# Performance work log

Hardware: AMD Instinct MI355X
Metric: run time of the kernel (lower is better)

The kernel has to match this reference:

```python
import jax, jax.numpy as jnp
import numpy as np

BLOCK_SIZE = 512
EPS = 1e-06


def setup_inputs() -> dict:
    key = jax.random.key(0)
    k1, k2, k3 = jax.random.split(key, 3)
    B, H, S, D = 2, 32, 4096, 128
    return {
        "query_states": jax.random.normal(k1, (B, H, S, D), dtype=jnp.float32),
        "key_states": jax.random.normal(k2, (B, H, S, D), dtype=jnp.float32),
        "value_states": jax.random.normal(k3, (B, H, S, D), dtype=jnp.float32),
        "phi_scale": jnp.ones((H, 1, D), dtype=jnp.float32),
        "phi_bias": jnp.zeros((H, 1, D), dtype=jnp.float32),
    }


def _feature_map(x, phi_scale, phi_bias):
    # x: (B, H, N, S_blk, D); scale/bias: (H, 1, D) -> broadcast over (B, N)
    y = x * phi_scale[None, :, None] + phi_bias[None, :, None]
    return jax.nn.elu(y) + 1.0


def reference(query_states, key_states, value_states, phi_scale, phi_bias):
    B, H, S, D = query_states.shape
    nb = (S + BLOCK_SIZE - 1) // BLOCK_SIZE
    pad = nb * BLOCK_SIZE - S
    if pad > 0:
        p = [(0, 0), (0, 0), (0, pad), (0, 0)]
        query_states = jnp.pad(query_states, p)
        key_states = jnp.pad(key_states, p)
        value_states = jnp.pad(value_states, p)
    q = query_states.reshape(B, H, nb, BLOCK_SIZE, D)
    k = key_states.reshape(B, H, nb, BLOCK_SIZE, D)
    v = value_states.reshape(B, H, nb, BLOCK_SIZE, D)
    phi_q = _feature_map(q, phi_scale, phi_bias)
    phi_k = _feature_map(k, phi_scale, phi_bias)
    # per-block KV aggregation: S_dm = sum_s phi_k[s,d] v[s,m]
    S_dm = jnp.einsum('bhnsd,bhnsm->bhndm', phi_k, v)
    Z = phi_k.sum(axis=-2)  # (B, H, nb, D)
    num = jnp.einsum('bhnsd,bhndm->bhnsm', phi_q, S_dm)
    den = jnp.einsum('bhnsd,bhnd->bhns', phi_q, Z)[..., None] + EPS
    out = (num / den).reshape(B, H, nb * BLOCK_SIZE, D)
    if pad > 0:
        out = out[:, :, :S, :]
    return out
```

## Files before the change

### kernel.cpp

```cpp
#include <hip/hip_runtime.h>
#include <cstdint>

#define NH 32
#define SEQ 4096
#define DDIM 128
#define BSZ 512
#define SKC 64
#define NCH 8
#define KT_STRIDE 33
#define ST_STRIDE 68
#define OFF_K0 0
#define OFF_V0 (128 * KT_STRIDE)
#define OFF_K1 (2 * 128 * KT_STRIDE)
#define OFF_V1 (3 * 128 * KT_STRIDE)
#define OFF_ST 0
#define OFF_QS0 (128 * ST_STRIDE)
#define OFF_QS1 (OFF_QS0 + 64 * ST_STRIDE)
#define OFF_Z   (OFF_QS1 + 64 * ST_STRIDE)
#define OFF_DEN0 (OFF_Z + 128)
#define OFF_DEN1 (OFF_DEN0 + 64)
#define LDS_DW (OFF_DEN1 + 64)

typedef _Float16 f16x8 __attribute__((ext_vector_type(8)));
typedef float f32x4 __attribute__((ext_vector_type(4)));

union FragU { uint32_t u[4]; f16x8 v; };

__device__ __forceinline__ float phi_fn(float x, float s, float b) {
    float y = fmaf(x, s, b);
    return y > 0.0f ? (y + 1.0f) : __expf(y);
}

__device__ __forceinline__ uint32_t pack_f16(float a, float b) {
    union { _Float16 h[2]; uint32_t u; } p;
    p.h[0] = (_Float16)a;
    p.h[1] = (_Float16)b;
    return p.u;
}

__global__ __launch_bounds__(256, 2) void linattn_kernel(
    const float* __restrict__ qg, const float* __restrict__ kg,
    const float* __restrict__ vg, const float* __restrict__ psg,
    const float* __restrict__ pbg, float* __restrict__ outg)
{
    __shared__ uint32_t lds[LDS_DW];
    float*    ldsf = (float*)lds;
    _Float16* ldsh = (_Float16*)lds;

    const int tid  = threadIdx.x;
    const int lane = tid & 63;
    const int wv   = tid >> 6;
    const int l15  = lane & 15;
    const int qd   = lane >> 4;

    const int gid = blockIdx.x;
    const int nb  = gid & 7;
    const int hh  = (gid >> 3) & 31;
    const int bb  = gid >> 8;

    const size_t base = ((size_t)(bb * NH + hh) * SEQ + (size_t)nb * BSZ) * DDIM;

    const int dp = tid & 63;
    const int qt = tid >> 6;
    const float2 sc2 = *(const float2*)(psg + hh * DDIM + 2 * dp);
    const float2 bi2 = *(const float2*)(pbg + hh * DDIM + 2 * dp);

    const int d4  = (tid & 31) * 4;
    const int sl2 = tid >> 5;
    const float4 sc4 = *(const float4*)(psg + hh * DDIM + d4);
    const float4 bi4 = *(const float4*)(pbg + hh * DDIM + d4);

    if (tid < 128) ldsf[OFF_Z + tid] = 0.0f;

    float z0 = 0.0f, z1 = 0.0f;

    f32x4 acc[2][8];
    #pragma unroll
    for (int a = 0; a < 2; ++a)
        #pragma unroll
        for (int c = 0; c < 8; ++c)
            acc[a][c] = (f32x4){0.f, 0.f, 0.f, 0.f};

    float2 kr[16], vr[16];
    const float* kbase = kg + base + 2 * dp;
    const float* vbase = vg + base + 2 * dp;

    auto loadkv = [&](int ch) {
        const size_t off = (size_t)(ch * SKC + qt * 16) * DDIM;
        #pragma unroll
        for (int j = 0; j < 16; ++j) {
            kr[j] = *(const float2*)(kbase + off + (size_t)j * DDIM);
            vr[j] = *(const float2*)(vbase + off + (size_t)j * DDIM);
        }
    };
    auto stagekv = [&](int buf) {
        uint32_t* bk = lds + (buf ? OFF_K1 : OFF_K0) + qt * 8;
        uint32_t* bv = lds + (buf ? OFF_V1 : OFF_V0) + qt * 8;
        const int r0 = (2 * dp) * KT_STRIDE;
        const int r1 = r0 + KT_STRIDE;
        #pragma unroll
        for (int j = 0; j < 8; ++j) {
            float p0x = phi_fn(kr[2*j].x,   sc2.x, bi2.x);
            float p1x = phi_fn(kr[2*j+1].x, sc2.x, bi2.x);
            float p0y = phi_fn(kr[2*j].y,   sc2.y, bi2.y);
            float p1y = phi_fn(kr[2*j+1].y, sc2.y, bi2.y);
            z0 += p0x + p1x;
            z1 += p0y + p1y;
            bk[r0 + j] = pack_f16(p0x, p1x);
            bk[r1 + j] = pack_f16(p0y, p1y);
            bv[r0 + j] = pack_f16(vr[2*j].x, vr[2*j+1].x);
            bv[r1 + j] = pack_f16(vr[2*j].y, vr[2*j+1].y);
        }
    };
    auto mfma1 = [&](int buf) {
        const int offK = buf ? OFF_K1 : OFF_K0;
        const int offV = buf ? OFF_V1 : OFF_V0;
        #pragma unroll
        for (int ks = 0; ks < 2; ++ks) {
            FragU af[2];
            #pragma unroll
            for (int tm = 0; tm < 2; ++tm) {
                const int m  = wv * 32 + tm * 16 + l15;
                const int ad = offV + m * KT_STRIDE + ks * 16 + qd * 4;
                af[tm].u[0] = lds[ad + 0]; af[tm].u[1] = lds[ad + 1];
                af[tm].u[2] = lds[ad + 2]; af[tm].u[3] = lds[ad + 3];
            }
            #pragma unroll
            for (int td = 0; td < 8; ++td) {
                const int dd = td * 16 + l15;
                const int bd = offK + dd * KT_STRIDE + ks * 16 + qd * 4;
                FragU bf;
                bf.u[0] = lds[bd + 0]; bf.u[1] = lds[bd + 1];
                bf.u[2] = lds[bd + 2]; bf.u[3] = lds[bd + 3];
                acc[0][td] = __builtin_amdgcn_mfma_f32_16x16x32_f16(af[0].v, bf.v, acc[0][td], 0, 0, 0);
                acc[1][td] = __builtin_amdgcn_mfma_f32_16x16x32_f16(af[1].v, bf.v, acc[1][td], 0, 0, 0);
            }
        }
    };

    loadkv(0);
    stagekv(0);
    loadkv(1);
    __syncthreads();
    for (int ch = 0; ch < NCH; ++ch) {
        if (ch + 1 < NCH) stagekv((ch + 1) & 1);
        if (ch + 2 < NCH) loadkv(ch + 2);
        mfma1(ch & 1);
        __syncthreads();
    }

    atomicAdd(&ldsf[OFF_Z + 2 * dp],     z0);
    atomicAdd(&ldsf[OFF_Z + 2 * dp + 1], z1);

    #pragma unroll
    for (int tm = 0; tm < 2; ++tm)
        #pragma unroll
        for (int td = 0; td < 8; ++td)
            #pragma unroll
            for (int r = 0; r < 4; ++r) {
                const int m  = wv * 32 + tm * 16 + qd * 4 + r;
                const int dd = td * 16 + l15;
                ldsh[m * (ST_STRIDE * 2) + dd] = (_Float16)acc[tm][td][r];
            }
    __syncthreads();

    const float4 zq = *(const float4*)(ldsf + OFF_Z + d4);

    float4 qr[8];
    const float* qbase = qg + base + d4;

    auto loadq = [&](int qc) {
        const size_t off = (size_t)(qc * SKC) * DDIM;
        #pragma unroll
        for (int i = 0; i < 8; ++i)
            qr[i] = *(const float4*)(qbase + off + (size_t)(sl2 + i * 8) * DDIM);
    };
    auto stageq = [&](int buf) {
        uint32_t* qsb  = lds  + (buf ? OFF_QS1  : OFF_QS0);
        float*    denb = ldsf + (buf ? OFF_DEN1 : OFF_DEN0);
        #pragma unroll
        for (int i = 0; i < 8; ++i) {
            const int srow = sl2 + i * 8;
            float p0 = phi_fn(qr[i].x, sc4.x, bi4.x);
            float p1 = phi_fn(qr[i].y, sc4.y, bi4.y);
            float p2 = phi_fn(qr[i].z, sc4.z, bi4.z);
            float p3 = phi_fn(qr[i].w, sc4.w, bi4.w);
            uint2 w;
            w.x = pack_f16(p0, p1);
            w.y = pack_f16(p2, p3);
            *(uint2*)(qsb + srow * ST_STRIDE + (tid & 31) * 2) = w;
            float pd = p0 * zq.x + p1 * zq.y + p2 * zq.z + p3 * zq.w;
            pd += __shfl_xor(pd, 16);
            pd += __shfl_xor(pd, 8);
            pd += __shfl_xor(pd, 4);
            pd += __shfl_xor(pd, 2);
            pd += __shfl_xor(pd, 1);
            if ((tid & 31) == 0) denb[srow] = pd;
        }
    };

    loadq(0);
    stageq(0);
    loadq(1);
    __syncthreads();

    for (int qc = 0; qc < 8; ++qc) {
        if (qc + 1 < 8) stageq((qc + 1) & 1);
        if (qc + 2 < 8) loadq(qc + 2);

        f32x4 acc2[8];
        #pragma unroll
        for (int c = 0; c < 8; ++c) acc2[c] = (f32x4){0.f, 0.f, 0.f, 0.f};

        const int qsOff  = (qc & 1) ? OFF_QS1  : OFF_QS0;
        const int denOff = (qc & 1) ? OFF_DEN1 : OFF_DEN0;

        #pragma unroll
        for (int ks = 0; ks < 4; ++ks) {
            const int srow = wv * 16 + l15;
            const int ad = qsOff + srow * ST_STRIDE + ks * 16 + qd * 4;
            FragU af;
            const uint4 t0 = *(const uint4*)(lds + ad);
            af.u[0] = t0.x; af.u[1] = t0.y; af.u[2] = t0.z; af.u[3] = t0.w;
            #pragma unroll
            for (int tn = 0; tn < 8; ++tn) {
                const int mm = tn * 16 + l15;
                const uint4 t1 = *(const uint4*)(lds + OFF_ST + mm * ST_STRIDE + ks * 16 + qd * 4);
                FragU bf;
                bf.u[0] = t1.x; bf.u[1] = t1.y; bf.u[2] = t1.z; bf.u[3] = t1.w;
                acc2[tn] = __builtin_amdgcn_mfma_f32_16x16x32_f16(af.v, bf.v, acc2[tn], 0, 0, 0);
            }
        }

        #pragma unroll
        for (int r = 0; r < 4; ++r) {
            const int srow = wv * 16 + qd * 4 + r;
            const float rden = 1.0f / (ldsf[denOff + srow] + 1e-6f);
            float* op = outg + base + (size_t)(qc * SKC + srow) * DDIM;
            #pragma unroll
            for (int tn = 0; tn < 8; ++tn)
                __builtin_nontemporal_store(acc2[tn][r] * rden, op + tn * 16 + l15);
        }
        if (qc + 1 < 8) __syncthreads();
    }
}

extern "C" void kernel_launch(void* const* d_in, const int* in_sizes, int n_in,
                              void* d_out, int out_size, void* d_ws, size_t ws_size,
                              hipStream_t stream) {
    const float* q  = (const float*)d_in[0];
    const float* k  = (const float*)d_in[1];
    const float* v  = (const float*)d_in[2];
    const float* ps = (const float*)d_in[3];
    const float* pb = (const float*)d_in[4];
    float* out = (float*)d_out;
    linattn_kernel<<<dim3(512), dim3(256), 0, stream>>>(q, k, v, ps, pb, out);
}
```

Baseline: 403.6 us.

## Use 512-thread blocks, swizzled K/V LDS layout, and register-direct Q phase

Block size goes from 256 to 512 threads, so each wave accumulates one 16-row tile of the K^T V product instead of two. The padded K/V LDS tiles become XOR-swizzled 32-dword rows with 128-bit stores and fragment loads. The Q phase no longer stages phi(q) in LDS: each wave loads its Q rows straight into MFMA fragments, computes the denominator with shuffles, and drops the per-chunk barriers and double buffering. The aim is more waves per CU, fewer LDS bank conflicts and instructions, and less synchronisation, at the cost of losing explicit prefetch of Q loads.

```diff
diff --git a/kernel.cpp b/kernel.cpp
--- a/kernel.cpp
+++ b/kernel.cpp
@@ -7,19 +7,17 @@
 #define BSZ 512
 #define SKC 64
 #define NCH 8
-#define KT_STRIDE 33
 #define ST_STRIDE 68
+
 #define OFF_K0 0
-#define OFF_V0 (128 * KT_STRIDE)
-#define OFF_K1 (2 * 128 * KT_STRIDE)
-#define OFF_V1 (3 * 128 * KT_STRIDE)
+#define OFF_V0 4096
+#define OFF_K1 8192
+#define OFF_V1 12288
 #define OFF_ST 0
-#define OFF_QS0 (128 * ST_STRIDE)
-#define OFF_QS1 (OFF_QS0 + 64 * ST_STRIDE)
-#define OFF_Z   (OFF_QS1 + 64 * ST_STRIDE)
-#define OFF_DEN0 (OFF_Z + 128)
-#define OFF_DEN1 (OFF_DEN0 + 64)
-#define LDS_DW (OFF_DEN1 + 64)
+#define OFF_Z  16384
+#define OFF_SC 16512
+#define OFF_SB 16640
+#define LDS_DW 16768
 
 typedef _Float16 f16x8 __attribute__((ext_vector_type(8)));
 typedef float f32x4 __attribute__((ext_vector_type(4)));
@@ -38,7 +36,7 @@
     return p.u;
 }
 
-__global__ __launch_bounds__(256, 2) void linattn_kernel(
+__global__ __launch_bounds__(512, 4) void linattn_kernel(
     const float* __restrict__ qg, const float* __restrict__ kg,
     const float* __restrict__ vg, const float* __restrict__ psg,
     const float* __restrict__ pbg, float* __restrict__ outg)
@@ -60,80 +58,83 @@
 
     const size_t base = ((size_t)(bb * NH + hh) * SEQ + (size_t)nb * BSZ) * DDIM;
 
-    const int dp = tid & 63;
-    const int qt = tid >> 6;
+    if (tid < 32) {
+        *(f32x4*)(ldsf + OFF_SC + tid * 4) = *(const f32x4*)(psg + hh * DDIM + tid * 4);
+    } else if (tid < 64) {
+        *(f32x4*)(ldsf + OFF_SB + (tid - 32) * 4) = *(const f32x4*)(pbg + hh * DDIM + (tid - 32) * 4);
+    }
+    if (tid < 128) ldsf[OFF_Z + tid] = 0.0f;
+
+    const int dp = lane;
     const float2 sc2 = *(const float2*)(psg + hh * DDIM + 2 * dp);
     const float2 bi2 = *(const float2*)(pbg + hh * DDIM + 2 * dp);
 
-    const int d4  = (tid & 31) * 4;
-    const int sl2 = tid >> 5;
-    const float4 sc4 = *(const float4*)(psg + hh * DDIM + d4);
-    const float4 bi4 = *(const float4*)(pbg + hh * DDIM + d4);
-
-    if (tid < 128) ldsf[OFF_Z + tid] = 0.0f;
-
     float z0 = 0.0f, z1 = 0.0f;
 
-    f32x4 acc[2][8];
+    f32x4 acc[8];
     #pragma unroll
-    for (int a = 0; a < 2; ++a)
-        #pragma unroll
-        for (int c = 0; c < 8; ++c)
-            acc[a][c] = (f32x4){0.f, 0.f, 0.f, 0.f};
-
-    float2 kr[16], vr[16];
+    for (int c = 0; c < 8; ++c) acc[c] = (f32x4){0.f, 0.f, 0.f, 0.f};
+
+    float2 kr[8], vr[8];
     const float* kbase = kg + base + 2 * dp;
     const float* vbase = vg + base + 2 * dp;
 
     auto loadkv = [&](int ch) {
-        const size_t off = (size_t)(ch * SKC + qt * 16) * DDIM;
-        #pragma unroll
-        for (int j = 0; j < 16; ++j) {
+        const size_t off = (size_t)(ch * SKC + wv * 8) * DDIM;
+        #pragma unroll
+        for (int j = 0; j < 8; ++j) {
             kr[j] = *(const float2*)(kbase + off + (size_t)j * DDIM);
             vr[j] = *(const float2*)(vbase + off + (size_t)j * DDIM);
         }
     };
+
     auto stagekv = [&](int buf) {
-        uint32_t* bk = lds + (buf ? OFF_K1 : OFF_K0) + qt * 8;
-        uint32_t* bv = lds + (buf ? OFF_V1 : OFF_V0) + qt * 8;
-        const int r0 = (2 * dp) * KT_STRIDE;
-        const int r1 = r0 + KT_STRIDE;
+        uint32_t* bk = lds + (buf ? OFF_K1 : OFF_K0);
+        uint32_t* bv = lds + (buf ? OFF_V1 : OFF_V0);
+        const int blk = ((wv ^ (dp & 7)) << 2);
+        uint32_t* k0 = bk + (2 * dp) * 32 + blk;
+        uint32_t* k1 = k0 + 32;
+        uint32_t* v0 = bv + (2 * dp) * 32 + blk;
+        uint32_t* v1 = v0 + 32;
+        float px[8], py[8];
         #pragma unroll
         for (int j = 0; j < 8; ++j) {
-            float p0x = phi_fn(kr[2*j].x,   sc2.x, bi2.x);
-            float p1x = phi_fn(kr[2*j+1].x, sc2.x, bi2.x);
-            float p0y = phi_fn(kr[2*j].y,   sc2.y, bi2.y);
-            float p1y = phi_fn(kr[2*j+1].y, sc2.y, bi2.y);
-            z0 += p0x + p1x;
-            z1 += p0y + p1y;
-            bk[r0 + j] = pack_f16(p0x, p1x);
-            bk[r1 + j] = pack_f16(p0y, p1y);
-            bv[r0 + j] = pack_f16(vr[2*j].x, vr[2*j+1].x);
-            bv[r1 + j] = pack_f16(vr[2*j].y, vr[2*j+1].y);
-        }
+            px[j] = phi_fn(kr[j].x, sc2.x, bi2.x);
+            py[j] = phi_fn(kr[j].y, sc2.y, bi2.y);
+            z0 += px[j];
+            z1 += py[j];
+        }
+        uint4 a;
+        a.x = pack_f16(px[0], px[1]); a.y = pack_f16(px[2], px[3]);
+        a.z = pack_f16(px[4], px[5]); a.w = pack_f16(px[6], px[7]);
+        *(uint4*)k0 = a;
+        a.x = pack_f16(py[0], py[1]); a.y = pack_f16(py[2], py[3]);
+        a.z = pack_f16(py[4], py[5]); a.w = pack_f16(py[6], py[7]);
+        *(uint4*)k1 = a;
+        a.x = pack_f16(vr[0].x, vr[1].x); a.y = pack_f16(vr[2].x, vr[3].x);
+        a.z = pack_f16(vr[4].x, vr[5].x); a.w = pack_f16(vr[6].x, vr[7].x);
+        *(uint4*)v0 = a;
+        a.x = pack_f16(vr[0].y, vr[1].y); a.y = pack_f16(vr[2].y, vr[3].y);
+        a.z = pack_f16(vr[4].y, vr[5].y); a.w = pack_f16(vr[6].y, vr[7].y);
+        *(uint4*)v1 = a;
     };
+
     auto mfma1 = [&](int buf) {
-        const int offK = buf ? OFF_K1 : OFF_K0;
-        const int offV = buf ? OFF_V1 : OFF_V0;
+        const uint32_t* bk = lds + (buf ? OFF_K1 : OFF_K0);
+        const uint32_t* bv = lds + (buf ? OFF_V1 : OFF_V0);
+        const int swz = (l15 >> 1) & 7;
         #pragma unroll
         for (int ks = 0; ks < 2; ++ks) {
-            FragU af[2];
-            #pragma unroll
-            for (int tm = 0; tm < 2; ++tm) {
-                const int m  = wv * 32 + tm * 16 + l15;
-                const int ad = offV + m * KT_STRIDE + ks * 16 + qd * 4;
-                af[tm].u[0] = lds[ad + 0]; af[tm].u[1] = lds[ad + 1];
-                af[tm].u[2] = lds[ad + 2]; af[tm].u[3] = lds[ad + 3];
-            }
+            const int coff = (((ks * 4 + qd) ^ swz) << 2);
+            FragU af;
+            const uint4 ta = *(const uint4*)(bv + (wv * 16 + l15) * 32 + coff);
+            af.u[0] = ta.x; af.u[1] = ta.y; af.u[2] = ta.z; af.u[3] = ta.w;
             #pragma unroll
             for (int td = 0; td < 8; ++td) {
-                const int dd = td * 16 + l15;
-                const int bd = offK + dd * KT_STRIDE + ks * 16 + qd * 4;
+                const uint4 tb = *(const uint4*)(bk + (td * 16 + l15) * 32 + coff);
                 FragU bf;
-                bf.u[0] = lds[bd + 0]; bf.u[1] = lds[bd + 1];
-                bf.u[2] = lds[bd + 2]; bf.u[3] = lds[bd + 3];
-                acc[0][td] = __builtin_amdgcn_mfma_f32_16x16x32_f16(af[0].v, bf.v, acc[0][td], 0, 0, 0);
-                acc[1][td] = __builtin_amdgcn_mfma_f32_16x16x32_f16(af[1].v, bf.v, acc[1][td], 0, 0, 0);
+                bf.u[0] = tb.x; bf.u[1] = tb.y; bf.u[2] = tb.z; bf.u[3] = tb.w;
+                acc[td] = __builtin_amdgcn_mfma_f32_16x16x32_f16(af.v, bf.v, acc[td], 0, 0, 0);
             }
         }
     };
@@ -153,95 +154,73 @@
     atomicAdd(&ldsf[OFF_Z + 2 * dp + 1], z1);
 
     #pragma unroll
-    for (int tm = 0; tm < 2; ++tm)
-        #pragma unroll
-        for (int td = 0; td < 8; ++td)
-            #pragma unroll
-            for (int r = 0; r < 4; ++r) {
-                const int m  = wv * 32 + tm * 16 + qd * 4 + r;
-                const int dd = td * 16 + l15;
-                ldsh[m * (ST_STRIDE * 2) + dd] = (_Float16)acc[tm][td][r];
+    for (int td = 0; td < 8; ++td)
+        #pragma unroll
+        for (int r = 0; r < 4; ++r)
+            ldsh[(wv * 16 + qd * 4 + r) * (ST_STRIDE * 2) + td * 16 + l15] = (_Float16)acc[td][r];
+
+    __syncthreads();
+
+    const float* qb = qg + base;
+    float* ob = outg + base;
+
+    #pragma unroll 1
+    for (int mt = 0; mt < 4; ++mt) {
+        const int rowA = wv * 64 + mt * 16 + l15;
+        const float* qrow = qb + (size_t)rowA * DDIM;
+
+        FragU af[4];
+        float den = 0.0f;
+        #pragma unroll
+        for (int ks = 0; ks < 4; ++ks) {
+            const int dofs = ks * 32 + qd * 8;
+            const f32x4 qa  = *(const f32x4*)(qrow + dofs);
+            const f32x4 qc  = *(const f32x4*)(qrow + dofs + 4);
+            const f32x4 sa  = *(const f32x4*)(ldsf + OFF_SC + dofs);
+            const f32x4 sb  = *(const f32x4*)(ldsf + OFF_SC + dofs + 4);
+            const f32x4 ba  = *(const f32x4*)(ldsf + OFF_SB + dofs);
+            const f32x4 bbv = *(const f32x4*)(ldsf + OFF_SB + dofs + 4);
+            const f32x4 za  = *(const f32x4*)(ldsf + OFF_Z + dofs);
+            const f32x4 zb  = *(const f32x4*)(ldsf + OFF_Z + dofs + 4);
+            float p[8];
+            #pragma unroll
+            for (int j = 0; j < 4; ++j) {
+                p[j]     = phi_fn(qa[j], sa[j], ba[j]);
+                p[4 + j] = phi_fn(qc[j], sb[j], bbv[j]);
+                den += p[j] * za[j] + p[4 + j] * zb[j];
             }
-    __syncthreads();
-
-    const float4 zq = *(const float4*)(ldsf + OFF_Z + d4);
-
-    float4 qr[8];
-    const float* qbase = qg + base + d4;
-
-    auto loadq = [&](int qc) {
-        const size_t off = (size_t)(qc * SKC) * DDIM;
-        #pragma unroll
-        for (int i = 0; i < 8; ++i)
-            qr[i] = *(const float4*)(qbase + off + (size_t)(sl2 + i * 8) * DDIM);
-    };
-    auto stageq = [&](int buf) {
-        uint32_t* qsb  = lds  + (buf ? OFF_QS1  : OFF_QS0);
-        float*    denb = ldsf + (buf ? OFF_DEN1 : OFF_DEN0);
-        #pragma unroll
-        for (int i = 0; i < 8; ++i) {
-            const int srow = sl2 + i * 8;
-            float p0 = phi_fn(qr[i].x, sc4.x, bi4.x);
-            float p1 = phi_fn(qr[i].y, sc4.y, bi4.y);
-            float p2 = phi_fn(qr[i].z, sc4.z, bi4.z);
-            float p3 = phi_fn(qr[i].w, sc4.w, bi4.w);
-            uint2 w;
-            w.x = pack_f16(p0, p1);
-            w.y = pack_f16(p2, p3);
-            *(uint2*)(qsb + srow * ST_STRIDE + (tid & 31) * 2) = w;
-            float pd = p0 * zq.x + p1 * zq.y + p2 * zq.z + p3 * zq.w;
-            pd += __shfl_xor(pd, 16);
-            pd += __shfl_xor(pd, 8);
-            pd += __shfl_xor(pd, 4);
-            pd += __shfl_xor(pd, 2);
-            pd += __shfl_xor(pd, 1);
-            if ((tid & 31) == 0) denb[srow] = pd;
-        }
-    };
-
-    loadq(0);
-    stageq(0);
-    loadq(1);
-    __syncthreads();
-
-    for (int qc = 0; qc < 8; ++qc) {
-        if (qc + 1 < 8) stageq((qc + 1) & 1);
-        if (qc + 2 < 8) loadq(qc + 2);
+            af[ks].u[0] = pack_f16(p[0], p[1]);
+            af[ks].u[1] = pack_f16(p[2], p[3]);
+            af[ks].u[2] = pack_f16(p[4], p[5]);
+            af[ks].u[3] = pack_f16(p[6], p[7]);
+        }
+        den += __shfl_xor(den, 16);
+        den += __shfl_xor(den, 32);
 
         f32x4 acc2[8];
         #pragma unroll
         for (int c = 0; c < 8; ++c) acc2[c] = (f32x4){0.f, 0.f, 0.f, 0.f};
 
-        const int qsOff  = (qc & 1) ? OFF_QS1  : OFF_QS0;
-        const int denOff = (qc & 1) ? OFF_DEN1 : OFF_DEN0;
-
         #pragma unroll
         for (int ks = 0; ks < 4; ++ks) {
-            const int srow = wv * 16 + l15;
-            const int ad = qsOff + srow * ST_STRIDE + ks * 16 + qd * 4;
-            FragU af;
-            const uint4 t0 = *(const uint4*)(lds + ad);
-            af.u[0] = t0.x; af.u[1] = t0.y; af.u[2] = t0.z; af.u[3] = t0.w;
             #pragma unroll
             for (int tn = 0; tn < 8; ++tn) {
-                const int mm = tn * 16 + l15;
-                const uint4 t1 = *(const uint4*)(lds + OFF_ST + mm * ST_STRIDE + ks * 16 + qd * 4);
+                const uint4 t1 = *(const uint4*)(lds + OFF_ST + (tn * 16 + l15) * ST_STRIDE + ks * 16 + qd * 4);
                 FragU bf;
                 bf.u[0] = t1.x; bf.u[1] = t1.y; bf.u[2] = t1.z; bf.u[3] = t1.w;
-                acc2[tn] = __builtin_amdgcn_mfma_f32_16x16x32_f16(af.v, bf.v, acc2[tn], 0, 0, 0);
+                acc2[tn] = __builtin_amdgcn_mfma_f32_16x16x32_f16(af[ks].v, bf.v, acc2[tn], 0, 0, 0);
             }
         }
 
         #pragma unroll
         for (int r = 0; r < 4; ++r) {
-            const int srow = wv * 16 + qd * 4 + r;
-            const float rden = 1.0f / (ldsf[denOff + srow] + 1e-6f);
-            float* op = outg + base + (size_t)(qc * SKC + srow) * DDIM;
+            const float dv = __shfl(den, qd * 4 + r);
+            const float rden = 1.0f / (dv + 1e-6f);
+            float* op = ob + (size_t)(wv * 64 + mt * 16 + qd * 4 + r) * DDIM;
             #pragma unroll
             for (int tn = 0; tn < 8; ++tn)
                 __builtin_nontemporal_store(acc2[tn][r] * rden, op + tn * 16 + l15);
         }
-        if (qc + 1 < 8) __syncthreads();
     }
 }
 
@@ -254,5 +233,5 @@
     const float* ps = (const float*)d_in[3];
     const float* pb = (const float*)d_in[4];
     float* out = (float*)d_out;
-    linattn_kernel<<<dim3(512), dim3(256), 0, stream>>>(q, k, v, ps, pb, out);
-}
+    linattn_kernel<<<dim3(512), dim3(512), 0, stream>>>(q, k, v, ps, pb, out);
+}
```

After: 522.8 us. 29.5% more time.
